# Kernel tuning notes

Hardware: AMD Instinct MI355X
Metric: run time of the kernel (lower is better)

The kernel has to match this reference:

```python
import jax, jax.numpy as jnp
import numpy as np
import math

NUM_HEADS = 8
WINDOW_SIZE = 1025
GLOBAL_TOKENS = 512  # effectively min(4, GLOBAL_TOKENS) indices are used, as in the torch code


def setup_inputs() -> dict:
    key = jax.random.key(0)
    k0, k1, k2 = jax.random.split(key, 3)
    B, C, H, W = 2, 256, 64, 64
    x = jax.random.normal(k0, (B, C, H, W), dtype=jnp.float32)
    # proj1: Linear(C, 3C); proj2: Linear(C, C). Stored as [in, out] matrices.
    w1 = jax.random.normal(k1, (C, 3 * C), dtype=jnp.float32) * 0.02
    b1 = jnp.zeros((3 * C,), dtype=jnp.float32)
    w2 = jax.random.normal(k2, (C, C), dtype=jnp.float32) * 0.02
    b2 = jnp.zeros((C,), dtype=jnp.float32)
    return {"x": x, "w1": w1, "b1": b1, "w2": w2, "b2": b2}


def _longformer_bias(L, W, window_size, global_tokens, dtype):
    # band: |i - j| <= window_size // 2  (matches start/end loop in torch code)
    i = jnp.arange(L)
    band = jnp.abs(i[:, None] - i[None, :]) <= (window_size // 2)
    gidx = [0, W - 1, L - W, L - 1][:global_tokens]
    g = jnp.zeros((L,), dtype=bool).at[jnp.array(gidx)].set(True)
    mask = band | g[:, None] | g[None, :]
    return jnp.where(mask, jnp.array(0.0, dtype), jnp.array(-jnp.inf, dtype))


def reference(x, w1, b1, w2, b2):
    B, C, H, W = x.shape
    L = H * W
    hd = C // NUM_HEADS
    # b c h w -> b (h w) c
    xt = x.reshape(B, C, L).transpose(0, 2, 1)
    qkv = xt @ w1 + b1  # [B, L, 3C]
    # 'b L (C H K)' with K=3, H=heads: last dim factors as (head_dim, heads, 3)
    qkv = qkv.reshape(B, L, hd, NUM_HEADS, 3).transpose(4, 0, 3, 1, 2)  # [3, B, Hh, L, hd]
    q, k, v = qkv[0], qkv[1], qkv[2]
    bias = _longformer_bias(L, W, WINDOW_SIZE, GLOBAL_TOKENS, x.dtype)
    scale = math.sqrt(hd)
    attn = jnp.einsum('bhqc,bhkc->bhqk', q, k) / scale + bias
    attn = jax.nn.softmax(attn, axis=-1)
    o = jnp.einsum('bhqk,bhkc->bhqc', attn, v)  # [B, Hh, L, hd]
    # 'b H (h w) C -> b h w (C H)': channel index = c*num_heads + head
    o = o.transpose(0, 2, 3, 1).reshape(B, H, W, hd * NUM_HEADS)
    out = o @ w2 + b2  # [B, H, W, C]
    return out.transpose(0, 3, 1, 2)  # b h w C -> b C h w
```

## Files before the change

kernel.cpp:

```cpp
#include <hip/hip_runtime.h>
#include <hip/hip_bf16.h>

#define BB 2
#define CC 256
#define HEADS 8
#define HD 32
#define LL 4096
#define HALF_WIN 512

using short8  = __attribute__((ext_vector_type(8))) short;
using short4v = __attribute__((ext_vector_type(4))) short;
using float4v = __attribute__((ext_vector_type(4))) float;

__device__ __forceinline__ ushort f2bf(float x) {
    uint u = __float_as_uint(x);
    u += 0x7fff + ((u >> 16) & 1);
    return (ushort)(u >> 16);
}
__device__ __forceinline__ float ubf(ushort u) {
    return __uint_as_float((uint)u << 16);
}
__device__ __forceinline__ uint pk2bf(float a, float b) {
#if __has_builtin(__builtin_amdgcn_cvt_pk_bf16_f32)
    typedef __bf16 v2bf __attribute__((ext_vector_type(2)));
    union { v2bf v; uint u; } cv;
    cv.v = __builtin_amdgcn_cvt_pk_bf16_f32(a, b);
    return cv.u;
#else
    return (uint)f2bf(a) | ((uint)f2bf(b) << 16);
#endif
}
__device__ __forceinline__ float rexp2(float x) {
#if __has_builtin(__builtin_amdgcn_exp2f)
    return __builtin_amdgcn_exp2f(x);
#else
    return exp2f(x);
#endif
}

#define QSCALE 0.25503485f

__global__ __launch_bounds__(256) void wt_kernel(const float* __restrict__ w1,
                                                 const float* __restrict__ w2,
                                                 ushort* __restrict__ w1t,
                                                 ushort* __restrict__ w2t) {
    __shared__ float tl[16][17];
    const int tx = threadIdx.x & 15, ty = threadIdx.x >> 4;
    const int ci0 = blockIdx.x * 16;
    const int y = blockIdx.y;
    if (y < 48) {
        int j0 = y * 16;
        tl[ty][tx] = w1[(size_t)(ci0 + ty) * 768 + j0 + tx];
        __syncthreads();
        w1t[(size_t)(j0 + ty) * CC + ci0 + tx] = f2bf(tl[tx][ty]);
    } else {
        int co0 = (y - 48) * 16;
        tl[ty][tx] = w2[(size_t)(ci0 + ty) * CC + co0 + tx];
        __syncthreads();
        w2t[(size_t)(co0 + ty) * CC + ci0 + tx] = f2bf(tl[tx][ty]);
    }
}

__global__ __launch_bounds__(256) void qkv_kernel(const float* __restrict__ x,
                                                  const ushort* __restrict__ w1t,
                                                  const float* __restrict__ b1,
                                                  ushort* __restrict__ qb,
                                                  ushort* __restrict__ kb,
                                                  ushort* __restrict__ vt) {
    __shared__ __align__(16) ushort xs[64 * 264];
    const int dg = blockIdx.x;
    const int l0 = blockIdx.y * 64;
    const int b  = blockIdx.z;
    const int t  = threadIdx.x;
    const int w  = t >> 6, ln = t & 63, c = ln & 15, g = ln >> 4;

    {
        const int l  = t & 63;
        const int cg = (t >> 6) * 4;
#pragma unroll
        for (int p = 0; p < 16; p++) {
            int c0 = p * 16 + cg;
            float a0 = x[((size_t)b * CC + c0 + 0) * LL + l0 + l];
            float a1 = x[((size_t)b * CC + c0 + 1) * LL + l0 + l];
            float a2 = x[((size_t)b * CC + c0 + 2) * LL + l0 + l];
            float a3 = x[((size_t)b * CC + c0 + 3) * LL + l0 + l];
            uint2 u;
            u.x = pk2bf(a0, a1);
            u.y = pk2bf(a2, a3);
            *(uint2*)&xs[l * 264 + c0] = u;
        }
    }
    __syncthreads();

    const int jbase = dg * 192 + w * 48;
    float4v acc[3][4] = {};
#pragma unroll
    for (int ks = 0; ks < 8; ks++) {
        short8 af[3], bfr[4];
#pragma unroll
        for (int jt = 0; jt < 3; jt++)
            af[jt] = *(const short8*)(w1t + (size_t)(jbase + jt * 16 + c) * CC + ks * 32 + g * 8);
#pragma unroll
        for (int lt = 0; lt < 4; lt++)
            bfr[lt] = *(const short8*)&xs[(lt * 16 + c) * 264 + ks * 32 + g * 8];
#pragma unroll
        for (int jt = 0; jt < 3; jt++)
#pragma unroll
            for (int lt = 0; lt < 4; lt++)
                acc[jt][lt] = __builtin_amdgcn_mfma_f32_16x16x32_bf16(af[jt], bfr[lt], acc[jt][lt], 0, 0, 0);
    }
    __syncthreads();

    ushort* qs  = xs;
    ushort* ksm = xs + 64 * 72;
    ushort* vs  = xs + 2 * 64 * 72;

#pragma unroll
    for (int jt = 0; jt < 3; jt++) {
#pragma unroll
        for (int r = 0; r < 4; r++) {
            int j = jbase + jt * 16 + g * 4 + r;
            float bias = b1[j];
            int t3 = j % 3, h = (j / 3) & 7, dl = (j / 24) & 7;
            int slot = h * 8 + dl;
            float v0 = acc[jt][0][r] + bias;
            float v1 = acc[jt][1][r] + bias;
            float v2 = acc[jt][2][r] + bias;
            float v3 = acc[jt][3][r] + bias;
            if (t3 == 0) { v0 *= QSCALE; v1 *= QSCALE; v2 *= QSCALE; v3 *= QSCALE; }
            uint u01 = pk2bf(v0, v1);
            uint u23 = pk2bf(v2, v3);
            ushort* dst = (t3 == 0) ? qs : (t3 == 1) ? ksm : vs;
            int stride = (t3 == 2) ? 74 : 72;
            dst[(0 * 16 + c) * stride + slot] = (ushort)u01;
            dst[(1 * 16 + c) * stride + slot] = (ushort)(u01 >> 16);
            dst[(2 * 16 + c) * stride + slot] = (ushort)u23;
            dst[(3 * 16 + c) * stride + slot] = (ushort)(u23 >> 16);
        }
    }
    __syncthreads();

    {
        const int l = t & 63;
#pragma unroll
        for (int p = 0; p < 2; p++) {
            int h = p * 4 + (t >> 6);
            size_t rowq = (((size_t)(b * 8 + h) * 4 + dg) * LL + l0 + l) * 8;
            *(short8*)(qb + rowq) = *(const short8*)&qs[l * 72 + h * 8];
            *(short8*)(kb + rowq) = *(const short8*)&ksm[l * 72 + h * 8];
        }
#pragma unroll
        for (int p = 0; p < 16; p++) {
            int hd = p * 4 + (t >> 6);
            vt[((size_t)(b * 8 + (hd >> 3)) * HD + dg * 8 + (hd & 7)) * LL + l0 + l] = vs[l * 74 + hd];
        }
    }
}

__device__ __forceinline__ int gcol_of(int tt) {
    return (tt == 0) ? 0 : (tt == 3) ? 63 : (tt == 252) ? LL - 64 : (tt == 255) ? LL - 1 : -1;
}

__global__ __launch_bounds__(256, 4) void attn_kernel(const ushort* __restrict__ qb,
                                                      const ushort* __restrict__ kb,
                                                      const ushort* __restrict__ vt,
                                                      ushort* __restrict__ obuf) {
    __shared__ __align__(16) ushort pshare[4][4][576];
    __shared__ float cbuf[4][3][64][9];
    const int n  = blockIdx.x;
    const int bh = ((n & 7) << 1) | ((n >> 3) & 1);
    const int it = n >> 4;
    const int i0 = it * 64;
    const int t  = threadIdx.x;
    const int w  = t >> 6;
    const int ln = t & 63;
    const int c  = ln & 15;
    const int g  = ln >> 4;

    const size_t slab = ((size_t)bh * 4 + g) * LL;

    short8 qf[4];
#pragma unroll
    for (int s = 0; s < 4; s++)
        qf[s] = *(const short8*)(qb + (slab + i0 + s * 16 + c) * 8);

    float4v o0[4], o1[4];
#pragma unroll
    for (int s = 0; s < 4; s++) {
#pragma unroll
        for (int r = 0; r < 4; r++) { o0[s][r] = 0.f; o1[s][r] = 0.f; }
    }
    float dsum[4] = {0.f, 0.f, 0.f, 0.f};

    int t0 = it * 4 - 32; if (t0 < 0) t0 = 0;
    int t1 = it * 4 + 35; if (t1 > 255) t1 = 255;
    int tf0 = it * 4 - 28; if (tf0 < 0) tf0 = 0;
    int tf1 = it * 4 + 31; if (tf1 > 255) tf1 = 255;

    int ml[12], nm = 0;
    for (int tt = t0; tt < tf0; tt++) ml[nm++] = tt;
    for (int tt = tf1 + 1; tt <= t1; tt++) ml[nm++] = tt;
    const int gt[4] = {0, 3, 252, 255};
#pragma unroll
    for (int e = 0; e < 4; e++)
        if (gt[e] < t0 || gt[e] > t1) ml[nm++] = gt[e];

    const ushort* vb = vt + (size_t)bh * HD * LL;
    ushort* wbb = &pshare[w][0][0];

    const int npair_f = (tf1 - tf0 + 1) >> 1;
    const int qq = npair_f >> 2, rem = npair_f & 3;
    const int mstart = w * qq + (w < rem ? w : rem);
    const int mcount = qq + (w < rem ? 1 : 0);
    const int tfs = tf0 + 2 * mstart;

    const ushort* kp  = kb + (slab + (size_t)(tfs * 16 + c)) * 8;
    const ushort* vp0 = vb + (size_t)c * LL + tfs * 16 + g * 8;
    const ushort* vp1 = vp0 + 16 * LL;
    for (int m = 0; m < mcount; m++) {
        const short8 kfA = *(const short8*)kp;
        const short8 kfB = *(const short8*)(kp + 128);
        kp += 256;
        const short8 v0f = *(const short8*)vp0;
        const short8 v1f = *(const short8*)vp1;
        vp0 += 32; vp1 += 32;
        float4v zero = {0.f, 0.f, 0.f, 0.f};
#pragma unroll
        for (int s = 0; s < 4; s++) {
            float4v sA = __builtin_amdgcn_mfma_f32_16x16x32_bf16(kfA, qf[s], zero, 0, 0, 0);
            float4v sB = __builtin_amdgcn_mfma_f32_16x16x32_bf16(kfB, qf[s], zero, 0, 0, 0);
            float pA[4], pB[4];
#pragma unroll
            for (int r = 0; r < 4; r++) { pA[r] = rexp2(sA[r]); dsum[s] += pA[r]; }
#pragma unroll
            for (int r = 0; r < 4; r++) { pB[r] = rexp2(sB[r]); dsum[s] += pB[r]; }
            uint2 ua, ub2;
            ua.x  = pk2bf(pA[0], pA[1]);
            ua.y  = pk2bf(pA[2], pA[3]);
            ub2.x = pk2bf(pB[0], pB[1]);
            ub2.y = pk2bf(pB[2], pB[3]);
            ushort* wb = wbb + s * 576;
            *(uint2*)&wb[c * 36 + 4 * g]      = ua;
            *(uint2*)&wb[c * 36 + 16 + 4 * g] = ub2;
        }
#pragma unroll
        for (int s = 0; s < 4; s++) {
            const ushort* wb = wbb + s * 576;
            union { short8 s8; short4v s4[2]; } pu;
            pu.s4[0] = *(const short4v*)&wb[c * 36 + 8 * g];
            pu.s4[1] = *(const short4v*)&wb[c * 36 + 8 * g + 4];
            o0[s] = __builtin_amdgcn_mfma_f32_16x16x32_bf16(pu.s8, v0f, o0[s], 0, 0, 0);
            o1[s] = __builtin_amdgcn_mfma_f32_16x16x32_bf16(pu.s8, v1f, o1[s], 0, 0, 0);
        }
    }

    for (int p = 0; p < (nm >> 1); p++) {
        if ((p & 3) != w) continue;
        const int tA = ml[2 * p], tB = ml[2 * p + 1];
        const int gA = gcol_of(tA), gB = gcol_of(tB);
        const short8 kfA = *(const short8*)(kb + (slab + (size_t)(tA * 16 + c)) * 8);
        const short8 kfB = *(const short8*)(kb + (slab + (size_t)(tB * 16 + c)) * 8);
        const int jv = (g < 2) ? tA * 16 + g * 8 : tB * 16 + (g - 2) * 8;
        const short8 v0f = *(const short8*)(vb + (size_t)c * LL + jv);
        const short8 v1f = *(const short8*)(vb + (size_t)(16 + c) * LL + jv);
        float4v zero = {0.f, 0.f, 0.f, 0.f};
#pragma unroll
        for (int s = 0; s < 4; s++) {
            const int i = i0 + s * 16 + c;
            float4v sA = __builtin_amdgcn_mfma_f32_16x16x32_bf16(kfA, qf[s], zero, 0, 0, 0);
            float4v sB = __builtin_amdgcn_mfma_f32_16x16x32_bf16(kfB, qf[s], zero, 0, 0, 0);
            float pA[4], pB[4];
#pragma unroll
            for (int r = 0; r < 4; r++) {
                int j = tA * 16 + g * 4 + r;
                bool ok = ((unsigned)(i - j + HALF_WIN) <= 2u * HALF_WIN) | (j == gA);
                pA[r] = ok ? rexp2(sA[r]) : 0.f;
                dsum[s] += pA[r];
            }
#pragma unroll
            for (int r = 0; r < 4; r++) {
                int j = tB * 16 + g * 4 + r;
                bool ok = ((unsigned)(i - j + HALF_WIN) <= 2u * HALF_WIN) | (j == gB);
                pB[r] = ok ? rexp2(sB[r]) : 0.f;
                dsum[s] += pB[r];
            }
            uint2 ua, ub2;
            ua.x  = pk2bf(pA[0], pA[1]);
            ua.y  = pk2bf(pA[2], pA[3]);
            ub2.x = pk2bf(pB[0], pB[1]);
            ub2.y = pk2bf(pB[2], pB[3]);
            ushort* wb = wbb + s * 576;
            *(uint2*)&wb[c * 36 + 4 * g]      = ua;
            *(uint2*)&wb[c * 36 + 16 + 4 * g] = ub2;
        }
#pragma unroll
        for (int s = 0; s < 4; s++) {
            const ushort* wb = wbb + s * 576;
            union { short8 s8; short4v s4[2]; } pu;
            pu.s4[0] = *(const short4v*)&wb[c * 36 + 8 * g];
            pu.s4[1] = *(const short4v*)&wb[c * 36 + 8 * g + 4];
            o0[s] = __builtin_amdgcn_mfma_f32_16x16x32_bf16(pu.s8, v0f, o0[s], 0, 0, 0);
            o1[s] = __builtin_amdgcn_mfma_f32_16x16x32_bf16(pu.s8, v1f, o1[s], 0, 0, 0);
        }
    }

#pragma unroll
    for (int s = 0; s < 4; s++) {
        if (s == w) continue;
        float* cb = &cbuf[s][(w < s) ? w : w - 1][ln][0];
#pragma unroll
        for (int r = 0; r < 4; r++) { cb[r] = o0[s][r]; cb[4 + r] = o1[s][r]; }
        cb[8] = dsum[s];
    }
    __syncthreads();

    float4v O0 = o0[w], O1 = o1[w];
    float ds = dsum[w];
#pragma unroll
    for (int k = 0; k < 3; k++) {
        const float* cb = &cbuf[w][k][ln][0];
#pragma unroll
        for (int r = 0; r < 4; r++) { O0[r] += cb[r]; O1[r] += cb[4 + r]; }
        ds += cb[8];
    }

    ds += __shfl_xor(ds, 16);
    ds += __shfl_xor(ds, 32);

    const int b = bh >> 3, hh = bh & 7;
#pragma unroll
    for (int r = 0; r < 4; r++) {
        float dn = __shfl(ds, g * 4 + r);
        float inv = 1.0f / dn;
        int irow = i0 + w * 16 + g * 4 + r;
        size_t rowb = ((size_t)b * LL + irow) * CC;
        obuf[rowb + (size_t)c * 8 + hh]        = f2bf(O0[r] * inv);
        obuf[rowb + (size_t)(16 + c) * 8 + hh] = f2bf(O1[r] * inv);
    }
}

__global__ __launch_bounds__(256) void attn_global_partial(const ushort* __restrict__ qb,
                                                           const ushort* __restrict__ kb,
                                                           const ushort* __restrict__ vt,
                                                           float* __restrict__ gpart) {
    __shared__ float qs[4][32];
    __shared__ float sc[4][256];
    const int ch = blockIdx.x;
    const int bh = blockIdx.y;
    const int t  = threadIdx.x;
    const int gidx[4] = {0, 63, LL - 64, LL - 1};

    if (t < 128) {
        int r = t >> 5, dd = t & 31;
        int i = gidx[r];
        qs[r][dd] = ubf(qb[(((size_t)bh * 4 + (dd >> 3)) * LL + i) * 8 + (dd & 7)]);
    }
    __syncthreads();

    const int j = ch * 256 + t;
    float dot[4] = {};
#pragma unroll
    for (int s = 0; s < 4; s++) {
        const short8 kf = *(const short8*)(kb + (((size_t)bh * 4 + s) * LL + j) * 8);
#pragma unroll
        for (int e = 0; e < 8; e++) {
            float kv = ubf((ushort)kf[e]);
#pragma unroll
            for (int r = 0; r < 4; r++) dot[r] += qs[r][s * 8 + e] * kv;
        }
    }
#pragma unroll
    for (int r = 0; r < 4; r++) sc[r][t] = rexp2(dot[r]);
    __syncthreads();

    const int w = t >> 6, ln = t & 63;
    float den = sc[w][ln] + sc[w][ln + 64] + sc[w][ln + 128] + sc[w][ln + 192];
#pragma unroll
    for (int o = 1; o < 64; o <<= 1) den += __shfl_xor(den, o);

    const int dd = ln & 31, half = ln >> 5;
    float acc = 0.f;
    const ushort* vrow = vt + ((size_t)bh * HD + dd) * LL + ch * 256 + half * 128;
#pragma unroll
    for (int q8 = 0; q8 < 16; q8++) {
        const short8 v8 = *(const short8*)(vrow + q8 * 8);
#pragma unroll
        for (int e = 0; e < 8; e++) acc += sc[w][half * 128 + q8 * 8 + e] * ubf((ushort)v8[e]);
    }
    acc += __shfl_xor(acc, 32);

    float* gp = gpart + (((size_t)bh * 16 + ch) * 4 + w) * 33;
    if (ln < 32) gp[dd] = acc;
    if (ln == 0) gp[32] = den;
}

__global__ __launch_bounds__(128) void attn_global_combine(const float* __restrict__ gpart,
                                                           ushort* __restrict__ obuf) {
    const int bh = blockIdx.x;
    const int t  = threadIdx.x;
    const int r  = t >> 5, dd = t & 31;
    const int gidx[4] = {0, 63, LL - 64, LL - 1};
    float pv = 0.f, den = 0.f;
#pragma unroll
    for (int ch = 0; ch < 16; ch++) {
        const float* gp = gpart + (((size_t)bh * 16 + ch) * 4 + r) * 33;
        pv  += gp[dd];
        den += gp[32];
    }
    const int b = bh >> 3, hh = bh & 7, i = gidx[r];
    obuf[((size_t)b * LL + i) * CC + dd * 8 + hh] = f2bf(pv / den);
}

__global__ __launch_bounds__(256) void proj_kernel(const ushort* __restrict__ obuf,
                                                   const ushort* __restrict__ w2t,
                                                   const float* __restrict__ b2,
                                                   float* __restrict__ out) {
    const int co0 = blockIdx.x * 16;
    const int l0  = blockIdx.y * 256 + (threadIdx.x >> 6) * 64;
    const int b   = blockIdx.z;
    const int ln  = threadIdx.x & 63;
    const int c   = ln & 15, g = ln >> 4;

    float4v acc[4] = {};
    const ushort* arow = w2t + (size_t)(co0 + c) * CC + g * 8;
    const ushort* brow = obuf + ((size_t)b * LL + l0 + c) * CC + g * 8;
#pragma unroll
    for (int ks = 0; ks < 8; ks++) {
        const short8 af = *(const short8*)(arow + ks * 32);
#pragma unroll
        for (int nf = 0; nf < 4; nf++) {
            const short8 bf = *(const short8*)(brow + (size_t)nf * 16 * CC + ks * 32);
            acc[nf] = __builtin_amdgcn_mfma_f32_16x16x32_bf16(af, bf, acc[nf], 0, 0, 0);
        }
    }
#pragma unroll
    for (int nf = 0; nf < 4; nf++) {
#pragma unroll
        for (int r = 0; r < 4; r++) {
            int co = co0 + g * 4 + r;
            int l  = l0 + nf * 16 + c;
            out[((size_t)b * CC + co) * LL + l] = acc[nf][r] + b2[co];
        }
    }
}

extern "C" void kernel_launch(void* const* d_in, const int* in_sizes, int n_in,
                              void* d_out, int out_size, void* d_ws, size_t ws_size,
                              hipStream_t stream) {
    const float* x  = (const float*)d_in[0];
    const float* w1 = (const float*)d_in[1];
    const float* b1 = (const float*)d_in[2];
    const float* w2 = (const float*)d_in[3];
    const float* b2 = (const float*)d_in[4];
    float* out = (float*)d_out;

    const size_t QKE = (size_t)BB * HEADS * LL * HD;
    const size_t OBE = (size_t)BB * LL * CC;
    ushort* qb  = (ushort*)d_ws;
    ushort* kb  = qb + QKE;
    ushort* vt  = kb + QKE;
    ushort* ob  = vt + QKE;
    float*  gp  = (float*)(ob + OBE);
    ushort* w2t = (ushort*)(gp + 16 * 16 * 4 * 33);
    ushort* w1t = w2t + CC * CC;

    wt_kernel<<<dim3(16, 64), 256, 0, stream>>>(w1, w2, w1t, w2t);
    qkv_kernel<<<dim3(4, 64, 2), 256, 0, stream>>>(x, w1t, b1, qb, kb, vt);
    attn_kernel<<<dim3(1024), 256, 0, stream>>>(qb, kb, vt, ob);
    attn_global_partial<<<dim3(16, 16), 256, 0, stream>>>(qb, kb, vt, gp);
    attn_global_combine<<<dim3(16), 128, 0, stream>>>(gp, ob);
    proj_kernel<<<dim3(16, 16, 2), 256, 0, stream>>>(ob, w2t, b2, out);
}
```

Measured before the change: 136.6 us.

## Merge global attention into windowed kernel, shrink tiles, prefetch K/V

Folds the global-token partial attention into the windowed attention kernel as 256 extra leading blocks, removing one launch. It also halves the row tiles of the QKV and output projection kernels to double the grid size, and software-prefetches the next K/V fragments in the windowed loop. It drops the occupancy hint of 4 blocks per SM from attention launch bounds, which may raise register use and lower occupancy. Smaller tiles in the GEMMs reduce weight reuse per block.

```diff
diff --git a/kernel.cpp b/kernel.cpp
--- a/kernel.cpp
+++ b/kernel.cpp
@@ -67,19 +67,19 @@
                                                   ushort* __restrict__ qb,
                                                   ushort* __restrict__ kb,
                                                   ushort* __restrict__ vt) {
-    __shared__ __align__(16) ushort xs[64 * 264];
+    __shared__ __align__(16) ushort xs[32 * 264];
     const int dg = blockIdx.x;
-    const int l0 = blockIdx.y * 64;
+    const int l0 = blockIdx.y * 32;
     const int b  = blockIdx.z;
     const int t  = threadIdx.x;
     const int w  = t >> 6, ln = t & 63, c = ln & 15, g = ln >> 4;
 
     {
-        const int l  = t & 63;
-        const int cg = (t >> 6) * 4;
-#pragma unroll
-        for (int p = 0; p < 16; p++) {
-            int c0 = p * 16 + cg;
+        const int l  = t & 31;
+        const int cG = (t >> 5) * 4;
+#pragma unroll
+        for (int p = 0; p < 8; p++) {
+            int c0 = p * 32 + cG;
             float a0 = x[((size_t)b * CC + c0 + 0) * LL + l0 + l];
             float a1 = x[((size_t)b * CC + c0 + 1) * LL + l0 + l];
             float a2 = x[((size_t)b * CC + c0 + 2) * LL + l0 + l];
@@ -93,27 +93,27 @@
     __syncthreads();
 
     const int jbase = dg * 192 + w * 48;
-    float4v acc[3][4] = {};
+    float4v acc[3][2] = {};
 #pragma unroll
     for (int ks = 0; ks < 8; ks++) {
-        short8 af[3], bfr[4];
+        short8 af[3], bfr[2];
 #pragma unroll
         for (int jt = 0; jt < 3; jt++)
             af[jt] = *(const short8*)(w1t + (size_t)(jbase + jt * 16 + c) * CC + ks * 32 + g * 8);
 #pragma unroll
-        for (int lt = 0; lt < 4; lt++)
+        for (int lt = 0; lt < 2; lt++)
             bfr[lt] = *(const short8*)&xs[(lt * 16 + c) * 264 + ks * 32 + g * 8];
 #pragma unroll
         for (int jt = 0; jt < 3; jt++)
 #pragma unroll
-            for (int lt = 0; lt < 4; lt++)
+            for (int lt = 0; lt < 2; lt++)
                 acc[jt][lt] = __builtin_amdgcn_mfma_f32_16x16x32_bf16(af[jt], bfr[lt], acc[jt][lt], 0, 0, 0);
     }
     __syncthreads();
 
     ushort* qs  = xs;
-    ushort* ksm = xs + 64 * 72;
-    ushort* vs  = xs + 2 * 64 * 72;
+    ushort* ksm = xs + 32 * 72;
+    ushort* vs  = xs + 2 * 32 * 72;
 
 #pragma unroll
     for (int jt = 0; jt < 3; jt++) {
@@ -125,33 +125,25 @@
             int slot = h * 8 + dl;
             float v0 = acc[jt][0][r] + bias;
             float v1 = acc[jt][1][r] + bias;
-            float v2 = acc[jt][2][r] + bias;
-            float v3 = acc[jt][3][r] + bias;
-            if (t3 == 0) { v0 *= QSCALE; v1 *= QSCALE; v2 *= QSCALE; v3 *= QSCALE; }
+            if (t3 == 0) { v0 *= QSCALE; v1 *= QSCALE; }
             uint u01 = pk2bf(v0, v1);
-            uint u23 = pk2bf(v2, v3);
             ushort* dst = (t3 == 0) ? qs : (t3 == 1) ? ksm : vs;
             int stride = (t3 == 2) ? 74 : 72;
-            dst[(0 * 16 + c) * stride + slot] = (ushort)u01;
-            dst[(1 * 16 + c) * stride + slot] = (ushort)(u01 >> 16);
-            dst[(2 * 16 + c) * stride + slot] = (ushort)u23;
-            dst[(3 * 16 + c) * stride + slot] = (ushort)(u23 >> 16);
+            dst[c * stride + slot]        = (ushort)u01;
+            dst[(16 + c) * stride + slot] = (ushort)(u01 >> 16);
         }
     }
     __syncthreads();
 
     {
-        const int l = t & 63;
-#pragma unroll
-        for (int p = 0; p < 2; p++) {
-            int h = p * 4 + (t >> 6);
-            size_t rowq = (((size_t)(b * 8 + h) * 4 + dg) * LL + l0 + l) * 8;
-            *(short8*)(qb + rowq) = *(const short8*)&qs[l * 72 + h * 8];
-            *(short8*)(kb + rowq) = *(const short8*)&ksm[l * 72 + h * 8];
-        }
-#pragma unroll
-        for (int p = 0; p < 16; p++) {
-            int hd = p * 4 + (t >> 6);
+        const int l = t & 31;
+        const int h = t >> 5;
+        size_t rowq = (((size_t)(b * 8 + h) * 4 + dg) * LL + l0 + l) * 8;
+        *(short8*)(qb + rowq) = *(const short8*)&qs[l * 72 + h * 8];
+        *(short8*)(kb + rowq) = *(const short8*)&ksm[l * 72 + h * 8];
+#pragma unroll
+        for (int p = 0; p < 8; p++) {
+            int hd = p * 8 + h;
             vt[((size_t)(b * 8 + (hd >> 3)) * HD + dg * 8 + (hd & 7)) * LL + l0 + l] = vs[l * 74 + hd];
         }
     }
@@ -161,17 +153,74 @@
     return (tt == 0) ? 0 : (tt == 3) ? 63 : (tt == 252) ? LL - 64 : (tt == 255) ? LL - 1 : -1;
 }
 
-__global__ __launch_bounds__(256, 4) void attn_kernel(const ushort* __restrict__ qb,
-                                                      const ushort* __restrict__ kb,
-                                                      const ushort* __restrict__ vt,
-                                                      ushort* __restrict__ obuf) {
-    __shared__ __align__(16) ushort pshare[4][4][576];
-    __shared__ float cbuf[4][3][64][9];
-    const int n  = blockIdx.x;
-    const int bh = ((n & 7) << 1) | ((n >> 3) & 1);
-    const int it = n >> 4;
+__global__ __launch_bounds__(256) void attn_kernel(const ushort* __restrict__ qb,
+                                                   const ushort* __restrict__ kb,
+                                                   const ushort* __restrict__ vt,
+                                                   ushort* __restrict__ obuf,
+                                                   float* __restrict__ gpart) {
+    __shared__ __align__(16) char smem[46080];
+    const int n = blockIdx.x;
+    const int t = threadIdx.x;
+
+    if (n < 256) {
+        float* qs = (float*)smem;
+        float* sc = qs + 128;
+        const int bh = ((n & 7) << 1) | ((n >> 3) & 1);
+        const int ch = n >> 4;
+        const int gidx[4] = {0, 63, LL - 64, LL - 1};
+
+        if (t < 128) {
+            int r = t >> 5, dd = t & 31;
+            int i = gidx[r];
+            qs[r * 32 + dd] = ubf(qb[(((size_t)bh * 4 + (dd >> 3)) * LL + i) * 8 + (dd & 7)]);
+        }
+        __syncthreads();
+
+        const int j = ch * 256 + t;
+        float dot[4] = {};
+#pragma unroll
+        for (int s = 0; s < 4; s++) {
+            const short8 kf = *(const short8*)(kb + (((size_t)bh * 4 + s) * LL + j) * 8);
+#pragma unroll
+            for (int e = 0; e < 8; e++) {
+                float kv = ubf((ushort)kf[e]);
+#pragma unroll
+                for (int r = 0; r < 4; r++) dot[r] += qs[r * 32 + s * 8 + e] * kv;
+            }
+        }
+#pragma unroll
+        for (int r = 0; r < 4; r++) sc[r * 256 + t] = rexp2(dot[r]);
+        __syncthreads();
+
+        const int w = t >> 6, ln = t & 63;
+        float den = sc[w * 256 + ln] + sc[w * 256 + ln + 64] +
+                    sc[w * 256 + ln + 128] + sc[w * 256 + ln + 192];
+#pragma unroll
+        for (int o = 1; o < 64; o <<= 1) den += __shfl_xor(den, o);
+
+        const int dd = ln & 31, half = ln >> 5;
+        float acc = 0.f;
+        const ushort* vrow = vt + ((size_t)bh * HD + dd) * LL + ch * 256 + half * 128;
+#pragma unroll
+        for (int q8 = 0; q8 < 16; q8++) {
+            const short8 v8 = *(const short8*)(vrow + q8 * 8);
+#pragma unroll
+            for (int e = 0; e < 8; e++) acc += sc[w * 256 + half * 128 + q8 * 8 + e] * ubf((ushort)v8[e]);
+        }
+        acc += __shfl_xor(acc, 32);
+
+        float* gp = gpart + (((size_t)bh * 16 + ch) * 4 + w) * 33;
+        if (ln < 32) gp[dd] = acc;
+        if (ln == 0) gp[32] = den;
+        return;
+    }
+
+    ushort* pshare = (ushort*)smem;
+    float*  cbuf   = (float*)(smem + 4 * 4 * 576 * 2);
+    const int nb = n - 256;
+    const int bh = ((nb & 7) << 1) | ((nb >> 3) & 1);
+    const int it = nb >> 4;
     const int i0 = it * 64;
-    const int t  = threadIdx.x;
     const int w  = t >> 6;
     const int ln = t & 63;
     const int c  = ln & 15;
@@ -206,7 +255,7 @@
         if (gt[e] < t0 || gt[e] > t1) ml[nm++] = gt[e];
 
     const ushort* vb = vt + (size_t)bh * HD * LL;
-    ushort* wbb = &pshare[w][0][0];
+    ushort* wbb = pshare + w * 4 * 576;
 
     const int npair_f = (tf1 - tf0 + 1) >> 1;
     const int qq = npair_f >> 2, rem = npair_f & 3;
@@ -217,13 +266,24 @@
     const ushort* kp  = kb + (slab + (size_t)(tfs * 16 + c)) * 8;
     const ushort* vp0 = vb + (size_t)c * LL + tfs * 16 + g * 8;
     const ushort* vp1 = vp0 + 16 * LL;
+
+    short8 kfA, kfB, v0f, v1f;
+    if (mcount > 0) {
+        kfA = *(const short8*)kp;
+        kfB = *(const short8*)(kp + 128);
+        v0f = *(const short8*)vp0;
+        v1f = *(const short8*)vp1;
+    }
     for (int m = 0; m < mcount; m++) {
-        const short8 kfA = *(const short8*)kp;
-        const short8 kfB = *(const short8*)(kp + 128);
-        kp += 256;
-        const short8 v0f = *(const short8*)vp0;
-        const short8 v1f = *(const short8*)vp1;
-        vp0 += 32; vp1 += 32;
+        const int adv = (m + 1 < mcount) ? 1 : 0;
+        const ushort* kp2  = kp  + adv * 256;
+        const ushort* vp02 = vp0 + adv * 32;
+        const ushort* vp12 = vp1 + adv * 32;
+        const short8 kfA2 = *(const short8*)kp2;
+        const short8 kfB2 = *(const short8*)(kp2 + 128);
+        const short8 v0f2 = *(const short8*)vp02;
+        const short8 v1f2 = *(const short8*)vp12;
+
         float4v zero = {0.f, 0.f, 0.f, 0.f};
 #pragma unroll
         for (int s = 0; s < 4; s++) {
@@ -252,23 +312,25 @@
             o0[s] = __builtin_amdgcn_mfma_f32_16x16x32_bf16(pu.s8, v0f, o0[s], 0, 0, 0);
             o1[s] = __builtin_amdgcn_mfma_f32_16x16x32_bf16(pu.s8, v1f, o1[s], 0, 0, 0);
         }
+        kfA = kfA2; kfB = kfB2; v0f = v0f2; v1f = v1f2;
+        kp = kp2; vp0 = vp02; vp1 = vp12;
     }
 
     for (int p = 0; p < (nm >> 1); p++) {
         if ((p & 3) != w) continue;
         const int tA = ml[2 * p], tB = ml[2 * p + 1];
         const int gA = gcol_of(tA), gB = gcol_of(tB);
-        const short8 kfA = *(const short8*)(kb + (slab + (size_t)(tA * 16 + c)) * 8);
-        const short8 kfB = *(const short8*)(kb + (slab + (size_t)(tB * 16 + c)) * 8);
+        const short8 mkA = *(const short8*)(kb + (slab + (size_t)(tA * 16 + c)) * 8);
+        const short8 mkB = *(const short8*)(kb + (slab + (size_t)(tB * 16 + c)) * 8);
         const int jv = (g < 2) ? tA * 16 + g * 8 : tB * 16 + (g - 2) * 8;
-        const short8 v0f = *(const short8*)(vb + (size_t)c * LL + jv);
-        const short8 v1f = *(const short8*)(vb + (size_t)(16 + c) * LL + jv);
+        const short8 mv0 = *(const short8*)(vb + (size_t)c * LL + jv);
+        const short8 mv1 = *(const short8*)(vb + (size_t)(16 + c) * LL + jv);
         float4v zero = {0.f, 0.f, 0.f, 0.f};
 #pragma unroll
         for (int s = 0; s < 4; s++) {
             const int i = i0 + s * 16 + c;
-            float4v sA = __builtin_amdgcn_mfma_f32_16x16x32_bf16(kfA, qf[s], zero, 0, 0, 0);
-            float4v sB = __builtin_amdgcn_mfma_f32_16x16x32_bf16(kfB, qf[s], zero, 0, 0, 0);
+            float4v sA = __builtin_amdgcn_mfma_f32_16x16x32_bf16(mkA, qf[s], zero, 0, 0, 0);
+            float4v sB = __builtin_amdgcn_mfma_f32_16x16x32_bf16(mkB, qf[s], zero, 0, 0, 0);
             float pA[4], pB[4];
 #pragma unroll
             for (int r = 0; r < 4; r++) {
@@ -299,15 +361,15 @@
             union { short8 s8; short4v s4[2]; } pu;
             pu.s4[0] = *(const short4v*)&wb[c * 36 + 8 * g];
             pu.s4[1] = *(const short4v*)&wb[c * 36 + 8 * g + 4];
-            o0[s] = __builtin_amdgcn_mfma_f32_16x16x32_bf16(pu.s8, v0f, o0[s], 0, 0, 0);
-            o1[s] = __builtin_amdgcn_mfma_f32_16x16x32_bf16(pu.s8, v1f, o1[s], 0, 0, 0);
+            o0[s] = __builtin_amdgcn_mfma_f32_16x16x32_bf16(pu.s8, mv0, o0[s], 0, 0, 0);
+            o1[s] = __builtin_amdgcn_mfma_f32_16x16x32_bf16(pu.s8, mv1, o1[s], 0, 0, 0);
         }
     }
 
 #pragma unroll
     for (int s = 0; s < 4; s++) {
         if (s == w) continue;
-        float* cb = &cbuf[s][(w < s) ? w : w - 1][ln][0];
+        float* cb = &cbuf[((s * 3 + ((w < s) ? w : w - 1)) * 64 + ln) * 9];
 #pragma unroll
         for (int r = 0; r < 4; r++) { cb[r] = o0[s][r]; cb[4 + r] = o1[s][r]; }
         cb[8] = dsum[s];
@@ -318,7 +380,7 @@
     float ds = dsum[w];
 #pragma unroll
     for (int k = 0; k < 3; k++) {
-        const float* cb = &cbuf[w][k][ln][0];
+        const float* cb = &cbuf[((w * 3 + k) * 64 + ln) * 9];
 #pragma unroll
         for (int r = 0; r < 4; r++) { O0[r] += cb[r]; O1[r] += cb[4 + r]; }
         ds += cb[8];
@@ -339,61 +401,6 @@
     }
 }
 
-__global__ __launch_bounds__(256) void attn_global_partial(const ushort* __restrict__ qb,
-                                                           const ushort* __restrict__ kb,
-                                                           const ushort* __restrict__ vt,
-                                                           float* __restrict__ gpart) {
-    __shared__ float qs[4][32];
-    __shared__ float sc[4][256];
-    const int ch = blockIdx.x;
-    const int bh = blockIdx.y;
-    const int t  = threadIdx.x;
-    const int gidx[4] = {0, 63, LL - 64, LL - 1};
-
-    if (t < 128) {
-        int r = t >> 5, dd = t & 31;
-        int i = gidx[r];
-        qs[r][dd] = ubf(qb[(((size_t)bh * 4 + (dd >> 3)) * LL + i) * 8 + (dd & 7)]);
-    }
-    __syncthreads();
-
-    const int j = ch * 256 + t;
-    float dot[4] = {};
-#pragma unroll
-    for (int s = 0; s < 4; s++) {
-        const short8 kf = *(const short8*)(kb + (((size_t)bh * 4 + s) * LL + j) * 8);
-#pragma unroll
-        for (int e = 0; e < 8; e++) {
-            float kv = ubf((ushort)kf[e]);
-#pragma unroll
-            for (int r = 0; r < 4; r++) dot[r] += qs[r][s * 8 + e] * kv;
-        }
-    }
-#pragma unroll
-    for (int r = 0; r < 4; r++) sc[r][t] = rexp2(dot[r]);
-    __syncthreads();
-
-    const int w = t >> 6, ln = t & 63;
-    float den = sc[w][ln] + sc[w][ln + 64] + sc[w][ln + 128] + sc[w][ln + 192];
-#pragma unroll
-    for (int o = 1; o < 64; o <<= 1) den += __shfl_xor(den, o);
-
-    const int dd = ln & 31, half = ln >> 5;
-    float acc = 0.f;
-    const ushort* vrow = vt + ((size_t)bh * HD + dd) * LL + ch * 256 + half * 128;
-#pragma unroll
-    for (int q8 = 0; q8 < 16; q8++) {
-        const short8 v8 = *(const short8*)(vrow + q8 * 8);
-#pragma unroll
-        for (int e = 0; e < 8; e++) acc += sc[w][half * 128 + q8 * 8 + e] * ubf((ushort)v8[e]);
-    }
-    acc += __shfl_xor(acc, 32);
-
-    float* gp = gpart + (((size_t)bh * 16 + ch) * 4 + w) * 33;
-    if (ln < 32) gp[dd] = acc;
-    if (ln == 0) gp[32] = den;
-}
-
 __global__ __launch_bounds__(128) void attn_global_combine(const float* __restrict__ gpart,
                                                            ushort* __restrict__ obuf) {
     const int bh = blockIdx.x;
@@ -416,30 +423,32 @@
                                                    const float* __restrict__ b2,
                                                    float* __restrict__ out) {
     const int co0 = blockIdx.x * 16;
-    const int l0  = blockIdx.y * 256 + (threadIdx.x >> 6) * 64;
+    const int w   = threadIdx.x >> 6;
+    const int l0  = blockIdx.y * 128 + (w >> 1) * 64;
+    const int nfb = (w & 1) * 2;
     const int b   = blockIdx.z;
     const int ln  = threadIdx.x & 63;
     const int c   = ln & 15, g = ln >> 4;
 
-    float4v acc[4] = {};
+    float4v acc[2] = {};
     const ushort* arow = w2t + (size_t)(co0 + c) * CC + g * 8;
     const ushort* brow = obuf + ((size_t)b * LL + l0 + c) * CC + g * 8;
 #pragma unroll
     for (int ks = 0; ks < 8; ks++) {
         const short8 af = *(const short8*)(arow + ks * 32);
 #pragma unroll
-        for (int nf = 0; nf < 4; nf++) {
-            const short8 bf = *(const short8*)(brow + (size_t)nf * 16 * CC + ks * 32);
-            acc[nf] = __builtin_amdgcn_mfma_f32_16x16x32_bf16(af, bf, acc[nf], 0, 0, 0);
-        }
-    }
-#pragma unroll
-    for (int nf = 0; nf < 4; nf++) {
+        for (int k = 0; k < 2; k++) {
+            const short8 bf = *(const short8*)(brow + (size_t)(nfb + k) * 16 * CC + ks * 32);
+            acc[k] = __builtin_amdgcn_mfma_f32_16x16x32_bf16(af, bf, acc[k], 0, 0, 0);
+        }
+    }
+#pragma unroll
+    for (int k = 0; k < 2; k++) {
 #pragma unroll
         for (int r = 0; r < 4; r++) {
             int co = co0 + g * 4 + r;
-            int l  = l0 + nf * 16 + c;
-            out[((size_t)b * CC + co) * LL + l] = acc[nf][r] + b2[co];
+            int l  = l0 + (nfb + k) * 16 + c;
+            out[((size_t)b * CC + co) * LL + l] = acc[k][r] + b2[co];
         }
     }
 }
@@ -465,9 +474,8 @@
     ushort* w1t = w2t + CC * CC;
 
     wt_kernel<<<dim3(16, 64), 256, 0, stream>>>(w1, w2, w1t, w2t);
-    qkv_kernel<<<dim3(4, 64, 2), 256, 0, stream>>>(x, w1t, b1, qb, kb, vt);
-    attn_kernel<<<dim3(1024), 256, 0, stream>>>(qb, kb, vt, ob);
-    attn_global_partial<<<dim3(16, 16), 256, 0, stream>>>(qb, kb, vt, gp);
+    qkv_kernel<<<dim3(4, 128, 2), 256, 0, stream>>>(x, w1t, b1, qb, kb, vt);
+    attn_kernel<<<dim3(1280), 256, 0, stream>>>(qb, kb, vt, ob, gp);
     attn_global_combine<<<dim3(16), 128, 0, stream>>>(gp, ob);
-    proj_kernel<<<dim3(16, 16, 2), 256, 0, stream>>>(ob, w2t, b2, out);
-}
+    proj_kernel<<<dim3(16, 32, 2), 256, 0, stream>>>(ob, w2t, b2, out);
+}
```

Measured after the change: 139.4 us. 1.02x slower.
